# Kernel optimization log

Hardware: AMD Instinct MI355X
Metric: run time of the kernel (lower is better)

The kernel has to match this reference:

```python
import jax, jax.numpy as jnp
import numpy as np

B, L, N, C = 4, 12, 1024, 3
D = 32          # num_hidden
ND = 32         # node_hidden
TE = 10         # time_emb_dim
ST = 96         # tsformer/st hidden feat
GH = 64         # estimation-gate hidden
KS = 2          # diffusion orders (k_s)
NUM_FEAT = 1
TID, DIW = 288, 7


def random_walk(adj):
    # adj: [B,N,N]; (D^-1)(A+I) row-normalized random-walk matrix
    n = adj.shape[-1]
    adj = adj + jnp.eye(n, dtype=adj.dtype)[None]
    d = adj.sum(axis=2)
    d_inv = jnp.where(d == 0, 0.0, 1.0 / d)
    return adj * d_inv[:, :, None]  # diag_embed(d_inv) @ adj == row scaling


def setup_inputs() -> dict:
    key = jax.random.key(0)
    ks = jax.random.split(key, 16)
    s = 0.05
    return {
        "history_data": jax.random.uniform(ks[0], (B, L, N, C), dtype=jnp.float32),
        "hidden_states_st": jax.random.normal(ks[1], (B, N, L, ST), dtype=jnp.float32),
        "sampled_adj": jax.random.uniform(ks[2], (B, N, N), dtype=jnp.float32),
        "W_emb": jax.random.normal(ks[3], (NUM_FEAT, D), dtype=jnp.float32) * s,
        "b_emb": jnp.zeros((D,), jnp.float32),
        "W_st": jax.random.normal(ks[4], (ST, D), dtype=jnp.float32) * s,
        "b_st": jnp.zeros((D,), jnp.float32),
        "TiD_emb": jax.random.normal(ks[5], (TID, TE), dtype=jnp.float32) * s,
        "DiW_emb": jax.random.normal(ks[6], (DIW, TE), dtype=jnp.float32) * s,
        "node_emb_u": jax.random.normal(ks[7], (N, ND), dtype=jnp.float32) * s,
        "node_emb_d": jax.random.normal(ks[8], (N, ND), dtype=jnp.float32) * s,
        "W_g1": jax.random.normal(ks[9], (2 * TE + 2 * ND, GH), dtype=jnp.float32) * s,
        "b_g1": jnp.zeros((GH,), jnp.float32),
        "W_g2": jax.random.normal(ks[10], (GH, 1), dtype=jnp.float32) * s,
        "b_g2": jnp.zeros((1,), jnp.float32),
        "W_dif": jax.random.normal(ks[11], ((1 + 3 * KS) * D, D), dtype=jnp.float32) * s,
        "b_dif": jnp.zeros((D,), jnp.float32),
    }


def reference(history_data, hidden_states_st, sampled_adj, W_emb, b_emb, W_st, b_st,
              TiD_emb, DiW_emb, node_emb_u, node_emb_d, W_g1, b_g1, W_g2, b_g2,
              W_dif, b_dif):
    # --- prepare inputs: time/node embedding gathers (D2STGNN._prepare_inputs) ---
    X = history_data.at[..., 2].multiply(1.0 / 7.0)
    t_idx = (X[..., NUM_FEAT] * TID).astype(jnp.int32)       # [B,L,N]
    d_idx = (X[..., NUM_FEAT + 1] * DIW).astype(jnp.int32)   # [B,L,N]
    T_D = TiD_emb[t_idx]   # [B,L,N,TE]
    D_W = DiW_emb[d_idx]   # [B,L,N,TE]
    Xf = X[..., :NUM_FEAT]  # [B,L,N,1]

    # --- graph construction (static self-adaptive + random-walk normalized learn graphs) ---
    static = jax.nn.softmax(jax.nn.relu(node_emb_d @ node_emb_u.T), axis=1)  # [N,N]
    rw_fwd = random_walk(sampled_adj)                       # [B,N,N]
    rw_bwd = random_walk(jnp.swapaxes(sampled_adj, -1, -2)) # [B,N,N]

    # --- input embedding + st hidden fusion ---
    H = jnp.einsum('blnf,fd->blnd', Xf, W_emb) + b_emb
    H_st = jnp.einsum('bnlk,kd->bnld', hidden_states_st, W_st) + b_st
    H = jax.nn.relu(H + jnp.transpose(H_st, (0, 2, 1, 3)))  # [B,L,N,D]

    # --- estimation (spatial) gate: sigmoid(FC(relu(FC([T_D,D_W,E_u,E_d])))) * X ---
    eu = jnp.broadcast_to(node_emb_u[None, None], (B, L, N, ND))
    ed = jnp.broadcast_to(node_emb_d[None, None], (B, L, N, ND))
    gate_feat = jnp.concatenate([T_D, D_W, eu, ed], axis=-1)  # [B,L,N,2TE+2ND]
    gate = jax.nn.sigmoid(jax.nn.relu(gate_feat @ W_g1 + b_g1) @ W_g2 + b_g2)  # [B,L,N,1]
    X_spa = H * gate

    # --- diffusion graph convolution over supports, KS orders each ---
    supports = [jnp.broadcast_to(static[None], (B, N, N)), rw_fwd, rw_bwd]
    outs = [X_spa]
    for A in supports:
        Z = X_spa
        for _ in range(KS):
            Z = jnp.einsum('bnm,blmd->blnd', A, Z)
            outs.append(Z)
    Hcat = jnp.concatenate(outs, axis=-1)  # [B,L,N,(1+3*KS)*D]
    out = Hcat @ W_dif + b_dif             # [B,L,N,D]
    return out
```

## Files before the change

### kernel.cpp

```cpp
#include <hip/hip_runtime.h>
#include <hip/hip_bf16.h>
#include <cstdint>

#define NN 1024
#define BBATCH 4
#define LLEN 12
#define NJ 384
#define TIDC 288
#define DIWC 7

typedef __attribute__((ext_vector_type(8))) short short8;
typedef __attribute__((ext_vector_type(4))) float f32x4;

__device__ inline ushort f2bf(float f) {
    unsigned u = __float_as_uint(f);
    u += 0x7FFFu + ((u >> 16) & 1u);
    return (ushort)(u >> 16);
}
__device__ inline float bf2f(ushort u) { return __uint_as_float(((unsigned)u) << 16); }

__global__ __launch_bounds__(256) void k_static(const float* __restrict__ emb_u,
                                                const float* __restrict__ emb_d,
                                                ushort* __restrict__ S_bf) {
    int i = blockIdx.x;
    int t = threadIdx.x;
    __shared__ float drow[32];
    __shared__ float red[256];
    if (t < 32) drow[t] = emb_d[i * 32 + t];
    __syncthreads();
    float v[4];
    float lsum = 0.f;
    for (int jj = 0; jj < 4; ++jj) {
        int j = jj * 256 + t;
        const float4* u4 = reinterpret_cast<const float4*>(emb_u + (size_t)j * 32);
        float acc = 0.f;
#pragma unroll
        for (int k4 = 0; k4 < 8; ++k4) {
            float4 u = u4[k4];
            acc += drow[k4 * 4 + 0] * u.x + drow[k4 * 4 + 1] * u.y +
                   drow[k4 * 4 + 2] * u.z + drow[k4 * 4 + 3] * u.w;
        }
        acc = fmaxf(acc, 0.f);
        v[jj] = __expf(acc);
        lsum += v[jj];
    }
    red[t] = lsum;
    __syncthreads();
    for (int s = 128; s > 0; s >>= 1) {
        if (t < s) red[t] += red[t + s];
        __syncthreads();
    }
    float inv = 1.f / red[0];
    for (int jj = 0; jj < 4; ++jj) S_bf[(size_t)i * NN + jj * 256 + t] = f2bf(v[jj] * inv);
}

__global__ __launch_bounds__(256) void k_adj_pre(const float* __restrict__ adj,
                                                 ushort* __restrict__ adjF,
                                                 ushort* __restrict__ adjT,
                                                 float* __restrict__ rs,
                                                 float* __restrict__ cs) {
    __shared__ float tile[64][65];
    int b = blockIdx.z;
    int r0 = blockIdx.y * 64, c0 = blockIdx.x * 64;
    int t = threadIdx.x;
    int col = (t & 15) * 4, rb = t >> 4;
#pragma unroll
    for (int i = 0; i < 4; ++i) {
        int r = rb + i * 16;
        float4 v = *reinterpret_cast<const float4*>(&adj[((size_t)b * NN + r0 + r) * NN + c0 + col]);
        tile[r][col] = v.x; tile[r][col + 1] = v.y; tile[r][col + 2] = v.z; tile[r][col + 3] = v.w;
        unsigned lo = (unsigned)f2bf(v.x) | ((unsigned)f2bf(v.y) << 16);
        unsigned hi = (unsigned)f2bf(v.z) | ((unsigned)f2bf(v.w) << 16);
        *reinterpret_cast<uint2*>(&adjF[((size_t)b * NN + r0 + r) * NN + c0 + col]) = make_uint2(lo, hi);
    }
    __syncthreads();
    {
        int r4 = t >> 2, q4 = t & 3;
        float s1 = 0.f;
#pragma unroll
        for (int c = 0; c < 16; ++c) s1 += tile[r4][q4 * 16 + c];
        s1 += __shfl_xor(s1, 1, 64);
        s1 += __shfl_xor(s1, 2, 64);
        if (q4 == 0) atomicAdd(&rs[b * NN + r0 + r4], s1);
        float s2 = 0.f;
#pragma unroll
        for (int rr = 0; rr < 16; ++rr) s2 += tile[q4 * 16 + rr][r4];
        s2 += __shfl_xor(s2, 1, 64);
        s2 += __shfl_xor(s2, 2, 64);
        if (q4 == 0) atomicAdd(&cs[b * NN + c0 + r4], s2);
    }
    int j = t >> 2, ch = t & 3;
    short8 o0, o1;
#pragma unroll
    for (int q = 0; q < 8; ++q) o0[q] = (short)f2bf(tile[ch * 16 + q][j]);
#pragma unroll
    for (int q = 0; q < 8; ++q) o1[q] = (short)f2bf(tile[ch * 16 + 8 + q][j]);
    size_t orow = ((size_t)b * NN + c0 + j) * NN + r0 + ch * 16;
    *(short8*)&adjT[orow] = o0;
    *(short8*)&adjT[orow + 8] = o1;
}

__global__ __launch_bounds__(64) void k_gate_pre(const float* __restrict__ emb_u,
                                                 const float* __restrict__ emb_d,
                                                 const float* __restrict__ W_g1,
                                                 const float* __restrict__ b_g1,
                                                 const float* __restrict__ TiD,
                                                 const float* __restrict__ DiW,
                                                 const float* __restrict__ W_st,
                                                 const float* __restrict__ W_dif,
                                                 float* __restrict__ U1, float* __restrict__ T1,
                                                 float* __restrict__ D1,
                                                 float* __restrict__ WstT_g,
                                                 float* __restrict__ W0T_g) {
    int r = blockIdx.x;
    int h = threadIdx.x;
    if (r < NN) {
        float acc = b_g1[h];
        for (int i = 0; i < 32; ++i) acc = fmaf(emb_u[r * 32 + i], W_g1[(20 + i) * 64 + h], acc);
        for (int i = 0; i < 32; ++i) acc = fmaf(emb_d[r * 32 + i], W_g1[(52 + i) * 64 + h], acc);
        U1[r * 64 + h] = acc;
    } else if (r < NN + TIDC) {
        int tt = r - NN;
        float acc = 0.f;
        for (int i = 0; i < 10; ++i) acc = fmaf(TiD[tt * 10 + i], W_g1[i * 64 + h], acc);
        T1[tt * 64 + h] = acc;
    } else if (r < NN + TIDC + DIWC) {
        int dd = r - (NN + TIDC);
        float acc = 0.f;
        for (int i = 0; i < 10; ++i) acc = fmaf(DiW[dd * 10 + i], W_g1[(10 + i) * 64 + h], acc);
        D1[dd * 64 + h] = acc;
    } else if (r == NN + TIDC + DIWC) {
        for (int i = h; i < 32 * 96; i += 64) WstT_g[i] = W_st[(i % 96) * 32 + i / 96];
    } else {
        for (int i = h; i < 32 * 32; i += 64) W0T_g[i] = W_dif[(i % 32) * 32 + i / 32];
    }
}

__global__ __launch_bounds__(256) void k_xspa(const float* __restrict__ hist,
                                              const float* __restrict__ hs,
                                              const float* __restrict__ W_emb,
                                              const float* __restrict__ b_emb,
                                              const float* __restrict__ b_st,
                                              const float* __restrict__ U1,
                                              const float* __restrict__ T1,
                                              const float* __restrict__ D1,
                                              const float* __restrict__ W_g2,
                                              const float* __restrict__ b_g2,
                                              const float* __restrict__ b_dif,
                                              const float* __restrict__ WstT_g,
                                              const float* __restrict__ W0T_g,
                                              ushort* __restrict__ XT,
                                              float* __restrict__ out) {
    __shared__ float WstT[32][100];
    __shared__ float W0T[32][36];
    __shared__ float hsm[64][96];
    __shared__ float Hs[64][36];
    __shared__ float gateL[64];
    __shared__ float histL[192];
    int t = threadIdx.x;
    int n0 = blockIdx.x * 64;
    int l = blockIdx.y;
    int b = blockIdx.z;
    for (int i = t; i < 32 * 96; i += 256) WstT[i / 96][i % 96] = WstT_g[i];
    for (int i = t; i < 32 * 32; i += 256) W0T[i / 32][i % 32] = W0T_g[i];
    if (t < 48)
        *(float4*)&histL[t * 4] =
            *(const float4*)&hist[(((size_t)b * LLEN + l) * NN + n0) * 3 + t * 4];
#pragma unroll
    for (int r = 0; r < 6; ++r) {
        int i = t + 256 * r;
        int s = i / 24, c = i % 24;
        float4 v = *(const float4*)&hs[(((size_t)b * NN + n0 + s) * LLEN + l) * 96 + c * 4];
        *(float4*)&hsm[s][c * 4] = v;
    }
    __syncthreads();
    int d = t & 31, g = t >> 5;
    float acc[8];
#pragma unroll
    for (int i = 0; i < 8; ++i) acc[i] = 0.f;
    for (int k4 = 0; k4 < 24; ++k4) {
        float4 w = *(const float4*)&WstT[d][k4 * 4];
#pragma unroll
        for (int i = 0; i < 8; ++i) {
            float4 h4 = *(const float4*)&hsm[g * 8 + i][k4 * 4];
            acc[i] = fmaf(h4.x, w.x, acc[i]);
            acc[i] = fmaf(h4.y, w.y, acc[i]);
            acc[i] = fmaf(h4.z, w.z, acc[i]);
            acc[i] = fmaf(h4.w, w.w, acc[i]);
        }
    }
    {
        float we = W_emb[d], be = b_emb[d], bst = b_st[d];
#pragma unroll
        for (int i = 0; i < 8; ++i) {
            int s = g * 8 + i;
            Hs[s][d] = fmaxf(fmaf(histL[s * 3], we, be) + bst + acc[i], 0.f);
        }
    }
    __syncthreads();
    {
        int s = t >> 2, q = t & 3;
        int n = n0 + s;
        float x1 = histL[s * 3 + 1];
        float x2 = histL[s * 3 + 2] * (1.f / 7.f);
        int ti = (int)(x1 * 288.f); ti = ti < 0 ? 0 : (ti > 287 ? 287 : ti);
        int di = (int)(x2 * 7.f);   di = di < 0 ? 0 : (di > 6 ? 6 : di);
        const float* up = U1 + n * 64 + q * 16;
        const float* tp = T1 + ti * 64 + q * 16;
        const float* dp = D1 + di * 64 + q * 16;
        const float* wp = W_g2 + q * 16;
        float a = 0.f;
#pragma unroll
        for (int h = 0; h < 16; ++h)
            a = fmaf(fmaxf(up[h] + tp[h] + dp[h], 0.f), wp[h], a);
        a += __shfl_xor(a, 1, 64);
        a += __shfl_xor(a, 2, 64);
        if (q == 0) gateL[s] = 1.f / (1.f + __expf(-(a + b_g2[0])));
    }
    __syncthreads();
    {
        float bd = b_dif[d];
#pragma unroll
        for (int i = 0; i < 8; ++i) {
            int s = g * 8 + i;
            float a = 0.f;
#pragma unroll
            for (int j4 = 0; j4 < 8; ++j4) {
                float4 w = *(const float4*)&W0T[d][j4 * 4];
                float4 h4 = *(const float4*)&Hs[s][j4 * 4];
                a = fmaf(h4.x, w.x, a); a = fmaf(h4.y, w.y, a);
                a = fmaf(h4.z, w.z, a); a = fmaf(h4.w, w.w, a);
            }
            out[(((size_t)b * LLEN + l) * NN + n0 + s) * 32 + d] = fmaf(gateL[s], a, bd);
        }
    }
    {
        int dd = t >> 3, c = t & 7;
        short8 v;
#pragma unroll
        for (int i = 0; i < 8; ++i) {
            int s = c * 8 + i;
            v[i] = (short)f2bf(Hs[s][dd] * gateL[s]);
        }
        *(short8*)&XT[((size_t)b * NJ + l * 32 + dd) * NN + n0 + c * 8] = v;
    }
}

#define DIFF_LOAD(ra, rw, kt)                                          \
    {                                                                  \
        const ushort* qA = pA + (size_t)(kt) * 64;                     \
        const ushort* qW = pW + (size_t)(kt) * 64;                     \
        _Pragma("unroll") for (int i = 0; i < 4; ++i)                  \
            ra[i] = *(const short8*)(qA + i * 8);                      \
        _Pragma("unroll") for (int i = 0; i < 2; ++i)                  \
            rw[i] = *(const short8*)(qW + i * 8);                      \
    }
#define DIFF_WRITE(buf, ra, rw)                                        \
    {                                                                  \
        _Pragma("unroll") for (int i = 0; i < 4; ++i)                  \
            *(short8*)&As[buf][arow * 64 + (((ac + i) ^ (arow & 7)) * 8)] = ra[i]; \
        _Pragma("unroll") for (int i = 0; i < 2; ++i)                  \
            *(short8*)&Ws[buf][wrow * 64 + (((wc + i) ^ (wrow & 7)) * 8)] = rw[i]; \
    }
#define DIFF_COMPUTE(buf)                                              \
    {                                                                  \
        _Pragma("unroll") for (int kk = 0; kk < 2; ++kk) {             \
            short8 af[4], bff[2];                                      \
            _Pragma("unroll") for (int mf = 0; mf < 4; ++mf) {         \
                int row = wm * 64 + mf * 16 + lr;                      \
                af[mf] = *(const short8*)&As[buf][row * 64 + (((kk * 4 + lg) ^ (row & 7)) * 8)]; \
            }                                                          \
            _Pragma("unroll") for (int nf = 0; nf < 2; ++nf) {         \
                int row = wn * 32 + nf * 16 + lr;                      \
                bff[nf] = *(const short8*)&Ws[buf][row * 64 + (((kk * 4 + lg) ^ (row & 7)) * 8)]; \
            }                                                          \
            _Pragma("unroll") for (int mf = 0; mf < 4; ++mf) {         \
                acc[mf][0] = __builtin_amdgcn_mfma_f32_16x16x32_bf16(af[mf], bff[0], acc[mf][0], 0, 0, 0); \
                acc[mf][1] = __builtin_amdgcn_mfma_f32_16x16x32_bf16(af[mf], bff[1], acc[mf][1], 0, 0, 0); \
            }                                                          \
        }                                                              \
    }

__global__ __launch_bounds__(256) void k_diff3(const ushort* __restrict__ S_bf,
                                               const ushort* __restrict__ adjF,
                                               const ushort* __restrict__ adjT,
                                               const float* __restrict__ rs,
                                               const float* __restrict__ cs,
                                               const ushort* __restrict__ In0,
                                               int in_per_chain,
                                               ushort* __restrict__ Out0) {
    __shared__ __align__(16) ushort As[2][128 * 64];
    __shared__ __align__(16) ushort Ws[2][64 * 64];
    int bid = blockIdx.x + 3 * blockIdx.y + 48 * blockIdx.z;
    int swz = (bid & 7) * 72 + (bid >> 3);
    int xx = swz % 3, yy = (swz / 3) % 16, zz = swz / 48;
    int s = zz >> 2, b = zz & 3;
    int j0 = xx * 128;
    int n0 = yy * 64;
    const size_t ZT = (size_t)BBATCH * NJ * NN;
    const ushort* Wb = (s == 0) ? S_bf
                     : (s == 1) ? adjF + (size_t)b * NN * NN
                                : adjT + (size_t)b * NN * NN;
    const float* deg = (s == 0) ? nullptr : (s == 1 ? rs : cs);
    const ushort* Inb = In0 + (in_per_chain ? (size_t)s * ZT : 0) + (size_t)b * NJ * NN;
    ushort* Outb = Out0 + (size_t)s * ZT + (size_t)b * NJ * NN;

    int t = threadIdx.x;
    int arow = t >> 1, ac = (t & 1) * 4;
    int wrow = t >> 2, wc = (t & 3) * 2;
    const ushort* pA = Inb + (size_t)(j0 + arow) * NN + ac * 8;
    const ushort* pW = Wb + (size_t)(n0 + wrow) * NN + wc * 8;
    int w = t >> 6, wm = w >> 1, wn = w & 1;
    int l = t & 63, lr = l & 15, lg = l >> 4;
    f32x4 acc[4][2];
#pragma unroll
    for (int i = 0; i < 4; ++i)
#pragma unroll
        for (int j = 0; j < 2; ++j) acc[i][j] = (f32x4){0.f, 0.f, 0.f, 0.f};

    short8 raA[4], rwA[2], raB[4], rwB[2];
    DIFF_LOAD(raA, rwA, 0);
    DIFF_LOAD(raB, rwB, 1);
    DIFF_WRITE(0, raA, rwA);
    __syncthreads();
    int cur = 0;
#pragma unroll 1
    for (int kt2 = 0; kt2 < 16; kt2 += 2) {
        if (kt2 + 2 < 16) DIFF_LOAD(raA, rwA, kt2 + 2);
        DIFF_COMPUTE(cur);
        DIFF_WRITE(cur ^ 1, raB, rwB);
        __syncthreads();
        cur ^= 1;
        if (kt2 + 3 < 16) DIFF_LOAD(raB, rwB, kt2 + 3);
        DIFF_COMPUTE(cur);
        if (kt2 + 2 < 16) DIFF_WRITE(cur ^ 1, raA, rwA);
        __syncthreads();
        cur ^= 1;
    }
    bool resid = (deg != nullptr);
#pragma unroll
    for (int nf = 0; nf < 2; ++nf) {
        int n_g = n0 + wn * 32 + nf * 16 + lr;
        float scale = 1.f;
        if (resid) scale = 1.f / (deg[b * NN + n_g] + 1.f);
#pragma unroll
        for (int mf = 0; mf < 4; ++mf) {
#pragma unroll
            for (int r = 0; r < 4; ++r) {
                int j_g = j0 + wm * 64 + mf * 16 + lg * 4 + r;
                float v = acc[mf][nf][r];
                if (resid) v += bf2f(Inb[(size_t)j_g * NN + n_g]);
                v *= scale;
                Outb[(size_t)j_g * NN + n_g] = f2bf(v);
            }
        }
    }
}

__global__ __launch_bounds__(256) void k_zall(const ushort* __restrict__ Z1,
                                              const ushort* __restrict__ Z2,
                                              const float* __restrict__ W_dif,
                                              float* __restrict__ out) {
    __shared__ float zs[6][32][64];
    __shared__ float wsm[6][32][32];
    const size_t ZT = (size_t)BBATCH * NJ * NN;
    int t = threadIdx.x;
    int n0 = blockIdx.x * 64;
    int l = blockIdx.y;
    int b = blockIdx.z;
    for (int i = t; i < 6144; i += 256) ((float*)wsm)[i] = W_dif[1024 + i];
    {
        int jr = t >> 3, ch = t & 7;
        size_t base = ((size_t)b * NJ + l * 32 + jr) * NN + n0 + ch * 8;
#pragma unroll
        for (int c = 0; c < 6; ++c) {
            const ushort* Zp = ((c & 1) ? Z2 : Z1) + (size_t)(c >> 1) * ZT;
            short8 v = *(const short8*)&Zp[base];
#pragma unroll
            for (int q = 0; q < 8; ++q) zs[c][jr][ch * 8 + q] = bf2f((ushort)v[q]);
        }
    }
    __syncthreads();
    int d = t & 31, nl = t >> 5;
    size_t ob = (((size_t)b * LLEN + l) * NN + n0 + nl) * 32 + d;
    float acc[8];
#pragma unroll
    for (int i = 0; i < 8; ++i) acc[i] = out[ob + (size_t)(8 * i) * 32];
#pragma unroll 2
    for (int c = 0; c < 6; ++c)
        for (int j = 0; j < 32; ++j) {
            float wv = wsm[c][j][d];
#pragma unroll
            for (int i = 0; i < 8; ++i) acc[i] = fmaf(zs[c][j][nl + 8 * i], wv, acc[i]);
        }
#pragma unroll
    for (int i = 0; i < 8; ++i) out[ob + (size_t)(8 * i) * 32] = acc[i];
}

extern "C" void kernel_launch(void* const* d_in, const int* in_sizes, int n_in,
                              void* d_out, int out_size, void* d_ws, size_t ws_size,
                              hipStream_t stream) {
    (void)in_sizes; (void)n_in; (void)out_size; (void)ws_size;
    const float* hist  = (const float*)d_in[0];
    const float* hs    = (const float*)d_in[1];
    const float* adj   = (const float*)d_in[2];
    const float* W_emb = (const float*)d_in[3];
    const float* b_emb = (const float*)d_in[4];
    const float* W_st  = (const float*)d_in[5];
    const float* b_st  = (const float*)d_in[6];
    const float* TiD   = (const float*)d_in[7];
    const float* DiW   = (const float*)d_in[8];
    const float* emb_u = (const float*)d_in[9];
    const float* emb_d = (const float*)d_in[10];
    const float* W_g1  = (const float*)d_in[11];
    const float* b_g1  = (const float*)d_in[12];
    const float* W_g2  = (const float*)d_in[13];
    const float* b_g2  = (const float*)d_in[14];
    const float* W_dif = (const float*)d_in[15];
    const float* b_dif = (const float*)d_in[16];
    float* out = (float*)d_out;

    uint8_t* w8 = (uint8_t*)d_ws;
    ushort* adjF = (ushort*)w8;
    ushort* adjT = (ushort*)(w8 + 8388608);
    ushort* S_bf = (ushort*)(w8 + 16777216);
    ushort* XT   = (ushort*)(w8 + 18874368);
    ushort* Z1   = (ushort*)(w8 + 22020096);
    ushort* Z2   = (ushort*)(w8 + 31457280);
    float*  rs   = (float*)(w8 + 40894464);
    float*  cs   = (float*)(w8 + 40910848);
    float*  U1   = (float*)(w8 + 40927232);
    float*  T1   = (float*)(w8 + 41189376);
    float*  D1   = (float*)(w8 + 41263104);
    float*  WstT = (float*)(w8 + 41264896);
    float*  W0T  = (float*)(w8 + 41277184);

    hipMemsetAsync(rs, 0, 2 * BBATCH * NN * sizeof(float), stream);
    k_adj_pre<<<dim3(16, 16, 4), 256, 0, stream>>>(adj, adjF, adjT, rs, cs);
    k_gate_pre<<<NN + TIDC + DIWC + 2, 64, 0, stream>>>(emb_u, emb_d, W_g1, b_g1, TiD, DiW,
                                                        W_st, W_dif, U1, T1, D1, WstT, W0T);
    k_static<<<NN, 256, 0, stream>>>(emb_u, emb_d, S_bf);
    k_xspa<<<dim3(16, 12, 4), 256, 0, stream>>>(hist, hs, W_emb, b_emb, b_st, U1, T1, D1,
                                                W_g2, b_g2, b_dif, WstT, W0T, XT, out);
    dim3 dgrid(3, 16, 12);
    k_diff3<<<dgrid, 256, 0, stream>>>(S_bf, adjF, adjT, rs, cs, XT, 0, Z1);
    k_diff3<<<dgrid, 256, 0, stream>>>(S_bf, adjF, adjT, rs, cs, Z1, 1, Z2);
    k_zall<<<dim3(16, 12, 4), 256, 0, stream>>>(Z1, Z2, W_dif, out);
}
```

Before: 241.2 us.

## Use bf16 MFMA for embedding projection and output W_dif projections

Replaces the scalar fp32 FMA loops in the X_spa kernel (hidden-state projection and first W_dif block) and in the final Z projection kernel with bf16 16x16x32 MFMA instructions. Weights are pre-transposed and converted to bf16 once, and Z tiles are transposed into LDS as bf16 without float expansion. The diffusion kernel's block-index swizzle decode is also reordered. This trades precision (bf16 inputs for the hidden projection and the H feeding XT) for far fewer ALU instructions and a smaller LDS footprint.

```diff
diff --git a/kernel.cpp b/kernel.cpp
--- a/kernel.cpp
+++ b/kernel.cpp
@@ -110,8 +110,8 @@
                                                  const float* __restrict__ W_dif,
                                                  float* __restrict__ U1, float* __restrict__ T1,
                                                  float* __restrict__ D1,
-                                                 float* __restrict__ WstT_g,
-                                                 float* __restrict__ W0T_g) {
+                                                 ushort* __restrict__ WstT_bf,
+                                                 ushort* __restrict__ WdT_bf) {
     int r = blockIdx.x;
     int h = threadIdx.x;
     if (r < NN) {
@@ -130,9 +130,9 @@
         for (int i = 0; i < 10; ++i) acc = fmaf(DiW[dd * 10 + i], W_g1[(10 + i) * 64 + h], acc);
         D1[dd * 64 + h] = acc;
     } else if (r == NN + TIDC + DIWC) {
-        for (int i = h; i < 32 * 96; i += 64) WstT_g[i] = W_st[(i % 96) * 32 + i / 96];
+        for (int i = h; i < 32 * 96; i += 64) WstT_bf[i] = f2bf(W_st[(i % 96) * 32 + i / 96]);
     } else {
-        for (int i = h; i < 32 * 32; i += 64) W0T_g[i] = W_dif[(i % 32) * 32 + i / 32];
+        for (int i = h; i < 32 * 224; i += 64) WdT_bf[i] = f2bf(W_dif[(i % 224) * 32 + i / 224]);
     }
 }
 
@@ -147,55 +147,39 @@
                                               const float* __restrict__ W_g2,
                                               const float* __restrict__ b_g2,
                                               const float* __restrict__ b_dif,
-                                              const float* __restrict__ WstT_g,
-                                              const float* __restrict__ W0T_g,
+                                              const ushort* __restrict__ WstT_bf,
+                                              const ushort* __restrict__ WdT_bf,
                                               ushort* __restrict__ XT,
                                               float* __restrict__ out) {
-    __shared__ float WstT[32][100];
-    __shared__ float W0T[32][36];
-    __shared__ float hsm[64][96];
-    __shared__ float Hs[64][36];
+    __shared__ __align__(16) ushort hsm[64][104];
+    __shared__ __align__(16) ushort Wst_s[32][104];
+    __shared__ __align__(16) ushort Hs_bf[64][40];
+    __shared__ __align__(16) ushort W0_s[32][40];
     __shared__ float gateL[64];
     __shared__ float histL[192];
     int t = threadIdx.x;
     int n0 = blockIdx.x * 64;
     int l = blockIdx.y;
     int b = blockIdx.z;
-    for (int i = t; i < 32 * 96; i += 256) WstT[i / 96][i % 96] = WstT_g[i];
-    for (int i = t; i < 32 * 32; i += 256) W0T[i / 32][i % 32] = W0T_g[i];
+    for (int i = t; i < 384; i += 256) {
+        int d = i / 12, c = i % 12;
+        *(short8*)&Wst_s[d][c * 8] = *(const short8*)&WstT_bf[d * 96 + c * 8];
+    }
+    if (t < 128) {
+        int d = t >> 2, c = t & 3;
+        *(short8*)&W0_s[d][c * 8] = *(const short8*)&WdT_bf[d * 224 + c * 8];
+    }
     if (t < 48)
         *(float4*)&histL[t * 4] =
             *(const float4*)&hist[(((size_t)b * LLEN + l) * NN + n0) * 3 + t * 4];
 #pragma unroll
-    for (int r = 0; r < 6; ++r) {
-        int i = t + 256 * r;
+    for (int rr = 0; rr < 6; ++rr) {
+        int i = t + 256 * rr;
         int s = i / 24, c = i % 24;
         float4 v = *(const float4*)&hs[(((size_t)b * NN + n0 + s) * LLEN + l) * 96 + c * 4];
-        *(float4*)&hsm[s][c * 4] = v;
-    }
-    __syncthreads();
-    int d = t & 31, g = t >> 5;
-    float acc[8];
-#pragma unroll
-    for (int i = 0; i < 8; ++i) acc[i] = 0.f;
-    for (int k4 = 0; k4 < 24; ++k4) {
-        float4 w = *(const float4*)&WstT[d][k4 * 4];
-#pragma unroll
-        for (int i = 0; i < 8; ++i) {
-            float4 h4 = *(const float4*)&hsm[g * 8 + i][k4 * 4];
-            acc[i] = fmaf(h4.x, w.x, acc[i]);
-            acc[i] = fmaf(h4.y, w.y, acc[i]);
-            acc[i] = fmaf(h4.z, w.z, acc[i]);
-            acc[i] = fmaf(h4.w, w.w, acc[i]);
-        }
-    }
-    {
-        float we = W_emb[d], be = b_emb[d], bst = b_st[d];
-#pragma unroll
-        for (int i = 0; i < 8; ++i) {
-            int s = g * 8 + i;
-            Hs[s][d] = fmaxf(fmaf(histL[s * 3], we, be) + bst + acc[i], 0.f);
-        }
+        ushort4 u;
+        u.x = f2bf(v.x); u.y = f2bf(v.y); u.z = f2bf(v.z); u.w = f2bf(v.w);
+        *(ushort4*)&hsm[s][c * 4] = u;
     }
     __syncthreads();
     {
@@ -211,27 +195,55 @@
         const float* wp = W_g2 + q * 16;
         float a = 0.f;
 #pragma unroll
-        for (int h = 0; h < 16; ++h)
-            a = fmaf(fmaxf(up[h] + tp[h] + dp[h], 0.f), wp[h], a);
+        for (int hh = 0; hh < 16; ++hh)
+            a = fmaf(fmaxf(up[hh] + tp[hh] + dp[hh], 0.f), wp[hh], a);
         a += __shfl_xor(a, 1, 64);
         a += __shfl_xor(a, 2, 64);
         if (q == 0) gateL[s] = 1.f / (1.f + __expf(-(a + b_g2[0])));
     }
-    __syncthreads();
+    int w = t >> 6, l6 = t & 63, lr = l6 & 15, lg = l6 >> 4;
+    f32x4 hacc[2];
+    hacc[0] = (f32x4){0.f, 0.f, 0.f, 0.f};
+    hacc[1] = (f32x4){0.f, 0.f, 0.f, 0.f};
+#pragma unroll
+    for (int kc = 0; kc < 3; ++kc) {
+        short8 a = *(const short8*)&hsm[w * 16 + lr][kc * 32 + lg * 8];
+        short8 b0 = *(const short8*)&Wst_s[lr][kc * 32 + lg * 8];
+        short8 b1 = *(const short8*)&Wst_s[16 + lr][kc * 32 + lg * 8];
+        hacc[0] = __builtin_amdgcn_mfma_f32_16x16x32_bf16(a, b0, hacc[0], 0, 0, 0);
+        hacc[1] = __builtin_amdgcn_mfma_f32_16x16x32_bf16(a, b1, hacc[1], 0, 0, 0);
+    }
+#pragma unroll
+    for (int h = 0; h < 2; ++h) {
+        int d = h * 16 + lr;
+        float we = W_emb[d];
+        float bb = b_emb[d] + b_st[d];
+#pragma unroll
+        for (int r = 0; r < 4; ++r) {
+            int s = w * 16 + lg * 4 + r;
+            float v = fmaxf(fmaf(histL[s * 3], we, bb) + hacc[h][r], 0.f);
+            Hs_bf[s][d] = f2bf(v);
+        }
+    }
+    __syncthreads();
+    f32x4 oacc[2];
+    oacc[0] = (f32x4){0.f, 0.f, 0.f, 0.f};
+    oacc[1] = (f32x4){0.f, 0.f, 0.f, 0.f};
     {
+        short8 a = *(const short8*)&Hs_bf[w * 16 + lr][lg * 8];
+        short8 b0 = *(const short8*)&W0_s[lr][lg * 8];
+        short8 b1 = *(const short8*)&W0_s[16 + lr][lg * 8];
+        oacc[0] = __builtin_amdgcn_mfma_f32_16x16x32_bf16(a, b0, oacc[0], 0, 0, 0);
+        oacc[1] = __builtin_amdgcn_mfma_f32_16x16x32_bf16(a, b1, oacc[1], 0, 0, 0);
+    }
+#pragma unroll
+    for (int h = 0; h < 2; ++h) {
+        int d = h * 16 + lr;
         float bd = b_dif[d];
 #pragma unroll
-        for (int i = 0; i < 8; ++i) {
-            int s = g * 8 + i;
-            float a = 0.f;
-#pragma unroll
-            for (int j4 = 0; j4 < 8; ++j4) {
-                float4 w = *(const float4*)&W0T[d][j4 * 4];
-                float4 h4 = *(const float4*)&Hs[s][j4 * 4];
-                a = fmaf(h4.x, w.x, a); a = fmaf(h4.y, w.y, a);
-                a = fmaf(h4.z, w.z, a); a = fmaf(h4.w, w.w, a);
-            }
-            out[(((size_t)b * LLEN + l) * NN + n0 + s) * 32 + d] = fmaf(gateL[s], a, bd);
+        for (int r = 0; r < 4; ++r) {
+            int s = w * 16 + lg * 4 + r;
+            out[(((size_t)b * LLEN + l) * NN + n0 + s) * 32 + d] = fmaf(gateL[s], oacc[h][r], bd);
         }
     }
     {
@@ -240,7 +252,7 @@
 #pragma unroll
         for (int i = 0; i < 8; ++i) {
             int s = c * 8 + i;
-            v[i] = (short)f2bf(Hs[s][dd] * gateL[s]);
+            v[i] = (short)f2bf(bf2f(Hs_bf[s][dd]) * gateL[s]);
         }
         *(short8*)&XT[((size_t)b * NJ + l * 32 + dd) * NN + n0 + c * 8] = v;
     }
@@ -293,7 +305,9 @@
     __shared__ __align__(16) ushort Ws[2][64 * 64];
     int bid = blockIdx.x + 3 * blockIdx.y + 48 * blockIdx.z;
     int swz = (bid & 7) * 72 + (bid >> 3);
-    int xx = swz % 3, yy = (swz / 3) % 16, zz = swz / 48;
+    int zz = swz / 48;
+    int rem = swz % 48;
+    int xx = rem >> 4, yy = rem & 15;
     int s = zz >> 2, b = zz & 3;
     int j0 = xx * 128;
     int n0 = yy * 64;
@@ -357,44 +371,54 @@
     }
 }
 
-__global__ __launch_bounds__(256) void k_zall(const ushort* __restrict__ Z1,
-                                              const ushort* __restrict__ Z2,
-                                              const float* __restrict__ W_dif,
-                                              float* __restrict__ out) {
-    __shared__ float zs[6][32][64];
-    __shared__ float wsm[6][32][32];
+__global__ __launch_bounds__(256) void k_zmfma(const ushort* __restrict__ Z1,
+                                               const ushort* __restrict__ Z2,
+                                               const ushort* __restrict__ WdT_bf,
+                                               float* __restrict__ out) {
+    __shared__ __align__(16) ushort zT[64][200];
+    __shared__ __align__(16) ushort Wd_s[32][200];
     const size_t ZT = (size_t)BBATCH * NJ * NN;
     int t = threadIdx.x;
     int n0 = blockIdx.x * 64;
     int l = blockIdx.y;
     int b = blockIdx.z;
-    for (int i = t; i < 6144; i += 256) ((float*)wsm)[i] = W_dif[1024 + i];
+    for (int i = t; i < 768; i += 256) {
+        int d = i / 24, c = i % 24;
+        *(short8*)&Wd_s[d][c * 8] = *(const short8*)&WdT_bf[d * 224 + 32 + c * 8];
+    }
     {
-        int jr = t >> 3, ch = t & 7;
-        size_t base = ((size_t)b * NJ + l * 32 + jr) * NN + n0 + ch * 8;
+        int j = t >> 3, ch = t & 7;
 #pragma unroll
         for (int c = 0; c < 6; ++c) {
             const ushort* Zp = ((c & 1) ? Z2 : Z1) + (size_t)(c >> 1) * ZT;
-            short8 v = *(const short8*)&Zp[base];
-#pragma unroll
-            for (int q = 0; q < 8; ++q) zs[c][jr][ch * 8 + q] = bf2f((ushort)v[q]);
-        }
-    }
-    __syncthreads();
-    int d = t & 31, nl = t >> 5;
-    size_t ob = (((size_t)b * LLEN + l) * NN + n0 + nl) * 32 + d;
-    float acc[8];
-#pragma unroll
-    for (int i = 0; i < 8; ++i) acc[i] = out[ob + (size_t)(8 * i) * 32];
-#pragma unroll 2
-    for (int c = 0; c < 6; ++c)
-        for (int j = 0; j < 32; ++j) {
-            float wv = wsm[c][j][d];
-#pragma unroll
-            for (int i = 0; i < 8; ++i) acc[i] = fmaf(zs[c][j][nl + 8 * i], wv, acc[i]);
-        }
-#pragma unroll
-    for (int i = 0; i < 8; ++i) out[ob + (size_t)(8 * i) * 32] = acc[i];
+            short8 v = *(const short8*)&Zp[((size_t)b * NJ + l * 32 + j) * NN + n0 + ch * 8];
+#pragma unroll
+            for (int q = 0; q < 8; ++q) zT[ch * 8 + q][c * 32 + j] = (ushort)v[q];
+        }
+    }
+    __syncthreads();
+    int w = t >> 6, l6 = t & 63, lr = l6 & 15, lg = l6 >> 4;
+    f32x4 acc[2];
+    acc[0] = (f32x4){0.f, 0.f, 0.f, 0.f};
+    acc[1] = (f32x4){0.f, 0.f, 0.f, 0.f};
+#pragma unroll
+    for (int kc = 0; kc < 6; ++kc) {
+        short8 a = *(const short8*)&zT[w * 16 + lr][kc * 32 + lg * 8];
+        short8 b0 = *(const short8*)&Wd_s[lr][kc * 32 + lg * 8];
+        short8 b1 = *(const short8*)&Wd_s[16 + lr][kc * 32 + lg * 8];
+        acc[0] = __builtin_amdgcn_mfma_f32_16x16x32_bf16(a, b0, acc[0], 0, 0, 0);
+        acc[1] = __builtin_amdgcn_mfma_f32_16x16x32_bf16(a, b1, acc[1], 0, 0, 0);
+    }
+#pragma unroll
+    for (int h = 0; h < 2; ++h) {
+        int d = h * 16 + lr;
+#pragma unroll
+        for (int r = 0; r < 4; ++r) {
+            int s = w * 16 + lg * 4 + r;
+            size_t oi = (((size_t)b * LLEN + l) * NN + n0 + s) * 32 + d;
+            out[oi] += acc[h][r];
+        }
+    }
 }
 
 extern "C" void kernel_launch(void* const* d_in, const int* in_sizes, int n_in,
@@ -432,18 +456,18 @@
     float*  U1   = (float*)(w8 + 40927232);
     float*  T1   = (float*)(w8 + 41189376);
     float*  D1   = (float*)(w8 + 41263104);
-    float*  WstT = (float*)(w8 + 41264896);
-    float*  W0T  = (float*)(w8 + 41277184);
+    ushort* WstT_bf = (ushort*)(w8 + 41264896);
+    ushort* WdT_bf  = (ushort*)(w8 + 41271040);
 
     hipMemsetAsync(rs, 0, 2 * BBATCH * NN * sizeof(float), stream);
     k_adj_pre<<<dim3(16, 16, 4), 256, 0, stream>>>(adj, adjF, adjT, rs, cs);
     k_gate_pre<<<NN + TIDC + DIWC + 2, 64, 0, stream>>>(emb_u, emb_d, W_g1, b_g1, TiD, DiW,
-                                                        W_st, W_dif, U1, T1, D1, WstT, W0T);
+                                                        W_st, W_dif, U1, T1, D1, WstT_bf, WdT_bf);
     k_static<<<NN, 256, 0, stream>>>(emb_u, emb_d, S_bf);
     k_xspa<<<dim3(16, 12, 4), 256, 0, stream>>>(hist, hs, W_emb, b_emb, b_st, U1, T1, D1,
-                                                W_g2, b_g2, b_dif, WstT, W0T, XT, out);
+                                                W_g2, b_g2, b_dif, WstT_bf, WdT_bf, XT, out);
     dim3 dgrid(3, 16, 12);
     k_diff3<<<dgrid, 256, 0, stream>>>(S_bf, adjF, adjT, rs, cs, XT, 0, Z1);
     k_diff3<<<dgrid, 256, 0, stream>>>(S_bf, adjF, adjT, rs, cs, Z1, 1, Z2);
-    k_zall<<<dim3(16, 12, 4), 256, 0, stream>>>(Z1, Z2, W_dif, out);
-}
+    k_zmfma<<<dim3(16, 12, 4), 256, 0, stream>>>(Z1, Z2, WdT_bf, out);
+}
```

Measured after the change: 211.5 us. -12.3%, faster.
